# Kernel tuning notes

Measured on AMD Instinct MI355X. Metric: run time of the kernel, lower is better.

Reference implementation:

```python
import jax, jax.numpy as jnp
import numpy as np

VOCAB, D = 32000, 1024
EPS = 1e-5

def setup_inputs() -> dict:
    key = jax.random.key(0)
    k1, k2, k3, k4 = jax.random.split(key, 4)
    patch_embeddings = jax.random.normal(k1, (16, 256, D), dtype=jnp.float32)
    text_prototypes = jax.random.normal(k2, (VOCAB, D), dtype=jnp.float32) * 0.02
    # nn.Linear(d, d): weight [d, d], bias [d]
    lim = 1.0 / np.sqrt(D)
    W = jax.random.uniform(k3, (D, D), minval=-lim, maxval=lim, dtype=jnp.float32)
    b = jax.random.uniform(k4, (D,), minval=-lim, maxval=lim, dtype=jnp.float32)
    gamma = jnp.ones((D,), dtype=jnp.float32)
    beta = jnp.zeros((D,), dtype=jnp.float32)
    return {"patch_embeddings": patch_embeddings, "text_prototypes": text_prototypes,
            "W": W, "b": b, "gamma": gamma, "beta": beta}

def _layer_norm(x, gamma, beta):
    mu = jnp.mean(x, axis=-1, keepdims=True)
    var = jnp.mean(jnp.square(x - mu), axis=-1, keepdims=True)
    return (x - mu) * jax.lax.rsqrt(var + EPS) * gamma + beta

def reference(patch_embeddings, text_prototypes, W, b, gamma, beta):
    # similarities: [B, P, V]
    sims = jnp.einsum('bpd,vd->bpv', patch_embeddings, text_prototypes)
    attn = jax.nn.softmax(sims, axis=-1)
    reprogrammed = jnp.einsum('bpv,vd->bpd', attn, text_prototypes)
    transformed = jnp.einsum('bpd,ed->bpe', reprogrammed, W) + b
    return _layer_norm(patch_embeddings + transformed, gamma, beta)
```

## Files before the change

### kernel.cpp

```cpp
#include <hip/hip_runtime.h>
#include <hip/hip_bf16.h>
#include <cstdint>
#include <cstddef>

#define D_DIM 1024
#define VOCAB 32000
#define ROWS  4096

typedef __attribute__((ext_vector_type(8))) short bf16x8;
typedef __attribute__((ext_vector_type(4))) float f32x4;
typedef __attribute__((ext_vector_type(4))) int   i32x4;
typedef __attribute__((ext_vector_type(8))) int   i32x8;

static __device__ __forceinline__ i32x8 cat8(i32x4 lo, i32x4 hi) {
  return __builtin_shufflevector(lo, hi, 0, 1, 2, 3, 4, 5, 6, 7);
}

static __device__ __forceinline__ unsigned short f2bf(float f) {
  union { float f; unsigned int u; } c; c.f = f;
  unsigned int u = c.u;
  u += 0x7fffu + ((u >> 16) & 1u);
  return (unsigned short)(u >> 16);
}

static __device__ __forceinline__ int pk8(float a, float b) {
  return __builtin_amdgcn_cvt_pk_fp8_f32(a, b, 0, false);
}

static __device__ __forceinline__ void gload_lds16(const void* g, void* s) {
  __builtin_amdgcn_global_load_lds(
      (const __attribute__((address_space(1))) uint32_t*)(g),
      (__attribute__((address_space(3))) uint32_t*)(s), 16, 0, 0);
}

__global__ void k_cvt(const float* __restrict__ src, short* __restrict__ dst, int n4) {
  int i = blockIdx.x * 256 + threadIdx.x;
  if (i < n4) {
    float4 v = *(const float4*)(src + (size_t)i * 4);
    ushort4 u;
    u.x = f2bf(v.x); u.y = f2bf(v.y); u.z = f2bf(v.z); u.w = f2bf(v.w);
    *(ushort4*)(dst + (size_t)i * 4) = u;
  }
}

__global__ void k_cvt_q8(const float* __restrict__ src, uint8_t* __restrict__ dst) {
  int i = blockIdx.x * 256 + threadIdx.x;
  float4 a = *(const float4*)(src + (size_t)i * 8);
  float4 b = *(const float4*)(src + (size_t)i * 8 + 4);
  uint2 o;
  o.x = (pk8(a.x, a.y) & 0xffff) | (pk8(a.z, a.w) << 16);
  o.y = (pk8(b.x, b.y) & 0xffff) | (pk8(b.z, b.w) << 16);
  *(uint2*)(dst + (size_t)i * 8) = o;
}

__global__ void k_prep_K8(const float* __restrict__ src, uint8_t* __restrict__ kb,
                          uint8_t* __restrict__ kt, int R, int C) {
  __shared__ uint8_t tile[64][68];
  int t  = threadIdx.x;
  int r0 = blockIdx.x * 64;
  int c0 = blockIdx.y * 64;
  int lr = t >> 4;
  int lc = (t & 15) * 4;
#pragma unroll
  for (int i = 0; i < 4; ++i) {
    int r = lr + 16 * i;
    float4 v = *(const float4*)(src + (size_t)(r0 + r) * C + c0 + lc);
    unsigned p = (pk8(v.x * 64.f, v.y * 64.f) & 0xffff) | (pk8(v.z * 64.f, v.w * 64.f) << 16);
    *(unsigned*)&tile[r][lc] = p;
    *(unsigned*)(kb + (size_t)(r0 + r) * C + c0 + lc) = p;
  }
  __syncthreads();
#pragma unroll
  for (int i = 0; i < 4; ++i) {
    int c = lr + 16 * i;
    unsigned p = tile[lc + 0][c] | (tile[lc + 1][c] << 8) |
                 (tile[lc + 2][c] << 16) | ((unsigned)tile[lc + 3][c] << 24);
    *(unsigned*)(kt + (size_t)(c0 + c) * R + r0 + lc) = p;
  }
}

#define PS8 144
#define G1NT 8
__global__ __launch_bounds__(256, 2) void k_g1(
    const uint8_t* __restrict__ A,
    const uint8_t* __restrict__ B,
    uint8_t* __restrict__ Pout, float* __restrict__ den)
{
  __shared__ uint8_t smem[65536];

  int tid  = threadIdx.x;
  int wave = tid >> 6;
  int lane = tid & 63;
  int quad = lane >> 4;
  int t16  = lane & 15;
  int wy = wave >> 1, wx = wave & 1;

  int swz = (blockIdx.x & 7) * 1000 + (blockIdx.x >> 3);
  int nt  = swz >> 5;
  int mt  = swz & 31;
  long mBase = (long)mt * 128;
  long nBase = (long)nt * 128;

  const uint8_t* Ab = A + (size_t)mBase * D_DIM;
  const uint8_t* Bb = B + (size_t)nBase * D_DIM;
  int lrow = lane >> 3;
  int lcol = ((lane & 7) ^ lrow) * 16;

  f32x4 acc[4][4];
#pragma unroll
  for (int i = 0; i < 4; ++i)
#pragma unroll
    for (int j = 0; j < 4; ++j) acc[i][j] = (f32x4){0.f, 0.f, 0.f, 0.f};

  int sw  = t16 & 7;
  int co0 = (((quad << 1) ^ sw) << 4);
  const int SC1 = 0x7F7F7F7F;

  auto STAGE = [&](int slot, int t) {
    uint8_t* As = &smem[slot * 32768];
    uint8_t* Bs = As + 16384;
    int kk = t * 128;
#pragma unroll
    for (int i = 0; i < 4; ++i) {
      int row = wave * 32 + i * 8;
      gload_lds16(Ab + (size_t)(row + lrow) * D_DIM + kk + lcol, As + row * 128);
      gload_lds16(Bb + (size_t)(row + lrow) * D_DIM + kk + lcol, Bs + row * 128);
    }
  };

  STAGE(0, 0);
  STAGE(1, 1);

  for (int t = 0; t < G1NT; ++t) {
    const uint8_t* As = &smem[(t & 1) * 32768];
    const uint8_t* Bs = As + 16384;

    if (t + 1 < G1NT)
      asm volatile("s_waitcnt vmcnt(8)\n\ts_barrier" ::: "memory");
    else
      asm volatile("s_waitcnt vmcnt(0)\n\ts_barrier" ::: "memory");

    i32x8 af[4], bfr[4];
#pragma unroll
    for (int mi = 0; mi < 4; ++mi) {
      const uint8_t* rp = &As[(wy * 64 + mi * 16 + t16) * 128];
      af[mi] = cat8(*(const i32x4*)(rp + co0), *(const i32x4*)(rp + (co0 ^ 16)));
    }
#pragma unroll
    for (int ni = 0; ni < 4; ++ni) {
      const uint8_t* rp = &Bs[(wx * 64 + ni * 16 + t16) * 128];
      bfr[ni] = cat8(*(const i32x4*)(rp + co0), *(const i32x4*)(rp + (co0 ^ 16)));
    }
    __builtin_amdgcn_s_setprio(1);
#pragma unroll
    for (int mi = 0; mi < 4; ++mi)
#pragma unroll
      for (int ni = 0; ni < 4; ++ni)
        acc[mi][ni] = __builtin_amdgcn_mfma_scale_f32_16x16x128_f8f6f4(
            af[mi], bfr[ni], acc[mi][ni], 0, 0, 0, SC1, 0, SC1);
    __builtin_amdgcn_s_setprio(0);
    asm volatile("s_barrier" ::: "memory");
    if (t + 2 < G1NT) STAGE(t & 1, t + 2);
  }

  float rsum[4][4];
#pragma unroll
  for (int mi = 0; mi < 4; ++mi)
#pragma unroll
    for (int r = 0; r < 4; ++r) rsum[mi][r] = 0.f;
#pragma unroll
  for (int mi = 0; mi < 4; ++mi) {
    int rloc = wy * 64 + mi * 16 + quad * 4;
#pragma unroll
    for (int ni = 0; ni < 4; ++ni) {
      int cloc = wx * 64 + ni * 16 + t16;
#pragma unroll
      for (int r = 0; r < 4; ++r) {
        float e = __expf(acc[mi][ni][r] * 0.015625f);
        smem[(rloc + r) * PS8 + cloc] = (uint8_t)pk8(e, e);
        rsum[mi][r] += e;
      }
    }
  }
#pragma unroll
  for (int mi = 0; mi < 4; ++mi)
#pragma unroll
    for (int r = 0; r < 4; ++r) {
      float s = rsum[mi][r];
      s += __shfl_xor(s, 1);
      s += __shfl_xor(s, 2);
      s += __shfl_xor(s, 4);
      s += __shfl_xor(s, 8);
      if (t16 == 0)
        atomicAdd(&den[mBase + wy * 64 + mi * 16 + quad * 4 + r], s);
    }
  __syncthreads();
  int rr  = tid >> 3;
  int c16 = (tid & 7) * 16;
#pragma unroll
  for (int i = 0; i < 4; ++i) {
    int row = i * 32 + rr;
    i32x4 v = *(const i32x4*)&smem[row * PS8 + c16];
    *(i32x4*)&Pout[(size_t)(mBase + row) * VOCAB + nBase + c16] = v;
  }
}

#define G2NT 125
__global__ __launch_bounds__(512, 2) void k_g2(
    const uint8_t* __restrict__ P, const uint8_t* __restrict__ KT,
    float* __restrict__ n0, float* __restrict__ n1)
{
  __shared__ uint8_t smem[98304];

  int tid  = threadIdx.x;
  int wave = tid >> 6;
  int lane = tid & 63;
  int quad = lane >> 4;
  int t16  = lane & 15;
  int wm = wave >> 2;
  int wn = wave & 3;

  int xn = blockIdx.x & 3;
  int zz = (blockIdx.x >> 2) & 1;
  int ym = blockIdx.x >> 3;
  long mBase = (long)ym * 128;
  long nBase = (long)xn * 256;
  int  k0    = zz * 16000;

  const uint8_t* Ab = P  + (size_t)mBase * VOCAB + k0;
  const uint8_t* Bb = KT + (size_t)nBase * VOCAB + k0;
  int lrow = lane >> 3;
  int lcol = ((lane & 7) ^ lrow) * 16;

  f32x4 acc[4][4];
#pragma unroll
  for (int i = 0; i < 4; ++i)
#pragma unroll
    for (int j = 0; j < 4; ++j) acc[i][j] = (f32x4){0.f, 0.f, 0.f, 0.f};

  int sw  = t16 & 7;
  int co0 = (((quad << 1) ^ sw) << 4);
  const int SC1 = 0x7F7F7F7F;

  auto STAGE = [&](int slot, int t) {
    uint8_t* As = &smem[slot * 49152];
    uint8_t* Bs = As + 16384;
    long kk = (long)t * 128;
#pragma unroll
    for (int g = 0; g < 2; ++g) {
      int r0 = wave * 16 + g * 8;
      gload_lds16(Ab + (size_t)(r0 + lrow) * VOCAB + kk + lcol, As + r0 * 128);
    }
#pragma unroll
    for (int g = 0; g < 4; ++g) {
      int r0 = wave * 32 + g * 8;
      gload_lds16(Bb + (size_t)(r0 + lrow) * VOCAB + kk + lcol, Bs + r0 * 128);
    }
  };

  STAGE(0, 0);
  STAGE(1, 1);

  for (int t = 0; t < G2NT; ++t) {
    const uint8_t* As = &smem[(t & 1) * 49152];
    const uint8_t* Bs = As + 16384;

    if (t + 1 < G2NT)
      asm volatile("s_waitcnt vmcnt(6)\n\ts_barrier" ::: "memory");
    else
      asm volatile("s_waitcnt vmcnt(0)\n\ts_barrier" ::: "memory");

    i32x8 af[4], bfr[4];
#pragma unroll
    for (int mi = 0; mi < 4; ++mi) {
      const uint8_t* rp = As + (wm * 64 + mi * 16 + t16) * 128;
      af[mi] = cat8(*(const i32x4*)(rp + co0), *(const i32x4*)(rp + (co0 ^ 16)));
    }
#pragma unroll
    for (int ni = 0; ni < 4; ++ni) {
      const uint8_t* rp = Bs + (wn * 64 + ni * 16 + t16) * 128;
      bfr[ni] = cat8(*(const i32x4*)(rp + co0), *(const i32x4*)(rp + (co0 ^ 16)));
    }
    __builtin_amdgcn_s_setprio(1);
#pragma unroll
    for (int mi = 0; mi < 4; ++mi)
#pragma unroll
      for (int ni = 0; ni < 4; ++ni)
        acc[mi][ni] = __builtin_amdgcn_mfma_scale_f32_16x16x128_f8f6f4(
            af[mi], bfr[ni], acc[mi][ni], 0, 0, 0, SC1, 0, SC1);
    __builtin_amdgcn_s_setprio(0);
    asm volatile("s_barrier" ::: "memory");
    if (t + 2 < G2NT) STAGE(t & 1, t + 2);
  }

  float* outp = zz ? n1 : n0;
#pragma unroll
  for (int mi = 0; mi < 4; ++mi) {
    long row = mBase + wm * 64 + mi * 16 + quad * 4;
#pragma unroll
    for (int ni = 0; ni < 4; ++ni) {
      long col = nBase + wn * 64 + ni * 16 + t16;
#pragma unroll
      for (int r = 0; r < 4; ++r)
        __builtin_nontemporal_store(acc[mi][ni][r],
                                    &outp[(size_t)(row + r) * D_DIM + col]);
    }
  }
}

__global__ __launch_bounds__(256) void k_gemm_bf(
    const short* __restrict__ A, int lda,
    const short* __restrict__ B, int ldb, int Kdim,
    const float* __restrict__ bias, const float* __restrict__ resid,
    float* __restrict__ Cout)
{
  __shared__ short smem[16384];
  short* As = smem;
  short* Bs = smem + 8192;

  int tid  = threadIdx.x;
  int wave = tid >> 6;
  int lane = tid & 63;
  int quad = lane >> 4;
  int t16  = lane & 15;
  int wy = wave >> 1, wx = wave & 1;

  long mBase = (long)blockIdx.y * 128;
  long nBase = (long)blockIdx.x * 128;

  const short* Ab = A + (size_t)mBase * lda;
  const short* Bb = B + (size_t)nBase * ldb;
  int lrow = lane >> 3;
  int lcol = ((lane & 7) ^ lrow) * 8;

  f32x4 acc[4][4];
#pragma unroll
  for (int i = 0; i < 4; ++i)
#pragma unroll
    for (int j = 0; j < 4; ++j) acc[i][j] = (f32x4){0.f, 0.f, 0.f, 0.f};

  int sw = t16 & 7;

  for (int kk = 0; kk < Kdim; kk += 64) {
#pragma unroll
    for (int i = 0; i < 4; ++i) {
      int row = wave * 32 + i * 8;
      gload_lds16(Ab + (size_t)(row + lrow) * lda + kk + lcol, &As[row * 64]);
      gload_lds16(Bb + (size_t)(row + lrow) * ldb + kk + lcol, &Bs[row * 64]);
    }
    __syncthreads();
#pragma unroll
    for (int kc = 0; kc < 8; kc += 4) {
      bf16x8 af[4], bfr[4];
#pragma unroll
      for (int mi = 0; mi < 4; ++mi)
        af[mi] = *(const bf16x8*)&As[(wy * 64 + mi * 16 + t16) * 64 +
                                     (((kc + quad) ^ sw) << 3)];
#pragma unroll
      for (int ni = 0; ni < 4; ++ni)
        bfr[ni] = *(const bf16x8*)&Bs[(wx * 64 + ni * 16 + t16) * 64 +
                                      (((kc + quad) ^ sw) << 3)];
#pragma unroll
      for (int mi = 0; mi < 4; ++mi)
#pragma unroll
        for (int ni = 0; ni < 4; ++ni)
          acc[mi][ni] = __builtin_amdgcn_mfma_f32_16x16x32_bf16(af[mi], bfr[ni],
                                                                acc[mi][ni], 0, 0, 0);
    }
    __syncthreads();
  }

#pragma unroll
  for (int mi = 0; mi < 4; ++mi) {
    long row = mBase + wy * 64 + mi * 16 + quad * 4;
#pragma unroll
    for (int ni = 0; ni < 4; ++ni) {
      long col = nBase + wx * 64 + ni * 16 + t16;
#pragma unroll
      for (int r = 0; r < 4; ++r) {
        size_t idx = (size_t)(row + r) * 1024 + col;
        Cout[idx] = acc[mi][ni][r] + bias[col] + resid[idx];
      }
    }
  }
}

__global__ void k_div(const float* __restrict__ n0, const float* __restrict__ n1,
                      const float* __restrict__ den, short* __restrict__ out) {
  int i = (blockIdx.x * 256 + threadIdx.x) * 4;
  float4 a = *(const float4*)(n0 + i);
  float4 b = *(const float4*)(n1 + i);
  float inv = 0.015625f / den[i >> 10];
  ushort4 u;
  u.x = f2bf((a.x + b.x) * inv); u.y = f2bf((a.y + b.y) * inv);
  u.z = f2bf((a.z + b.z) * inv); u.w = f2bf((a.w + b.w) * inv);
  *(ushort4*)(out + i) = u;
}

__global__ __launch_bounds__(256) void k_ln(const float* __restrict__ x,
                                            const float* __restrict__ gamma,
                                            const float* __restrict__ beta,
                                            float* __restrict__ out) {
  __shared__ float s_sum[4], s_sq[4];
  int row = blockIdx.x;
  int tid = threadIdx.x;
  const float* xr = x + (size_t)row * 1024;
  float4 v = *(const float4*)(xr + tid * 4);
  float s = v.x + v.y + v.z + v.w;
  float q = v.x * v.x + v.y * v.y + v.z * v.z + v.w * v.w;
#pragma unroll
  for (int off = 32; off >= 1; off >>= 1) {
    s += __shfl_down(s, off);
    q += __shfl_down(q, off);
  }
  int wv = tid >> 6;
  if ((tid & 63) == 0) { s_sum[wv] = s; s_sq[wv] = q; }
  __syncthreads();
  float tot  = s_sum[0] + s_sum[1] + s_sum[2] + s_sum[3];
  float totq = s_sq[0] + s_sq[1] + s_sq[2] + s_sq[3];
  float mu   = tot * (1.0f / 1024.0f);
  float var  = totq * (1.0f / 1024.0f) - mu * mu;
  float rstd = rsqrtf(var + 1e-5f);
  float4 g = *(const float4*)(gamma + tid * 4);
  float4 b = *(const float4*)(beta + tid * 4);
  float4 o;
  o.x = (v.x - mu) * rstd * g.x + b.x;
  o.y = (v.y - mu) * rstd * g.y + b.y;
  o.z = (v.z - mu) * rstd * g.z + b.z;
  o.w = (v.w - mu) * rstd * g.w + b.w;
  *(float4*)(out + (size_t)row * 1024 + tid * 4) = o;
}

extern "C" void kernel_launch(void* const* d_in, const int* in_sizes, int n_in,
                              void* d_out, int out_size, void* d_ws, size_t ws_size,
                              hipStream_t stream) {
  const float* patch = (const float*)d_in[0];
  const float* proto = (const float*)d_in[1];
  const float* W     = (const float*)d_in[2];
  const float* bvec  = (const float*)d_in[3];
  const float* gamma = (const float*)d_in[4];
  const float* beta  = (const float*)d_in[5];
  float* out = (float*)d_out;

  char* ws = (char*)d_ws;
  size_t off = 0;
  uint8_t* Q8  = (uint8_t*)(ws + off); off += (size_t)ROWS * D_DIM;
  uint8_t* Kb8 = (uint8_t*)(ws + off); off += (size_t)VOCAB * D_DIM;
  uint8_t* KT8 = (uint8_t*)(ws + off); off += (size_t)VOCAB * D_DIM;
  short*   Wb  = (short*)(ws + off);   off += (size_t)D_DIM * D_DIM * 2;
  short*   Rb  = (short*)(ws + off);   off += (size_t)ROWS * D_DIM * 2;
  uint8_t* P8  = (uint8_t*)(ws + off); off += (size_t)ROWS * VOCAB;
  float*   num = (float*)(ws + off);   off += (size_t)ROWS * D_DIM * 4;
  float*   den = (float*)(ws + off);   off += (size_t)ROWS * 4;
  float*   pre = (float*)P8;
  float*   nz0 = (float*)Kb8;
  float*   nz1 = num;

  hipMemsetAsync(den, 0, ROWS * sizeof(float), stream);

  k_cvt_q8<<<ROWS * D_DIM / 8 / 256, 256, 0, stream>>>(patch, Q8);
  k_cvt<<<D_DIM * D_DIM / 4 / 256, 256, 0, stream>>>(W, Wb, D_DIM * D_DIM / 4);
  k_prep_K8<<<dim3(VOCAB / 64, D_DIM / 64), 256, 0, stream>>>(proto, Kb8, KT8, VOCAB, D_DIM);

  k_g1<<<8000, 256, 0, stream>>>(Q8, Kb8, P8, den);

  k_g2<<<256, 512, 0, stream>>>(P8, KT8, nz0, nz1);

  k_div<<<ROWS * D_DIM / 4 / 256, 256, 0, stream>>>(nz0, nz1, den, Rb);

  k_gemm_bf<<<dim3(D_DIM / 128, ROWS / 128), 256, 0, stream>>>(
      Rb, D_DIM, Wb, D_DIM, D_DIM, bvec, patch, pre);

  k_ln<<<ROWS, 256, 0, stream>>>(pre, gamma, beta, out);
}
```

Baseline: 647.6 us.

## Retile second GEMM to 128x128 blocks with 256 threads and 512 CTAs

The P·K^T GEMM moves from 128x256 tiles with 8 waves to 128x128 tiles with 4 waves, each wave still computing 64x64, and launches 512 blocks instead of 256. Block-index decomposition is reordered so split-K halves sit in the high bits and the D tiles are innermost. The aim is better occupancy and load balance across CUs with smaller LDS per block, at the cost of more global reloads of the A tile. Stores in k_g1's P output become nontemporal, and k_g2's output stores become regular.

Result: slower. 662.3 us (+2.3%).

```diff
diff --git a/kernel.cpp b/kernel.cpp
--- a/kernel.cpp
+++ b/kernel.cpp
@@ -201,34 +201,34 @@
   for (int i = 0; i < 4; ++i) {
     int row = i * 32 + rr;
     i32x4 v = *(const i32x4*)&smem[row * PS8 + c16];
-    *(i32x4*)&Pout[(size_t)(mBase + row) * VOCAB + nBase + c16] = v;
+    __builtin_nontemporal_store(v, (i32x4*)&Pout[(size_t)(mBase + row) * VOCAB + nBase + c16]);
   }
 }
 
 #define G2NT 125
-__global__ __launch_bounds__(512, 2) void k_g2(
+__global__ __launch_bounds__(256, 2) void k_g2(
     const uint8_t* __restrict__ P, const uint8_t* __restrict__ KT,
     float* __restrict__ n0, float* __restrict__ n1)
 {
-  __shared__ uint8_t smem[98304];
+  __shared__ uint8_t smem[65536];
 
   int tid  = threadIdx.x;
   int wave = tid >> 6;
   int lane = tid & 63;
   int quad = lane >> 4;
   int t16  = lane & 15;
-  int wm = wave >> 2;
-  int wn = wave & 3;
-
-  int xn = blockIdx.x & 3;
-  int zz = (blockIdx.x >> 2) & 1;
-  int ym = blockIdx.x >> 3;
-  long mBase = (long)ym * 128;
-  long nBase = (long)xn * 256;
+  int wy = wave >> 1, wx = wave & 1;
+
+  int bid = blockIdx.x;
+  int zz  = bid >> 8;
+  int dt  = bid & 7;
+  int mt  = (bid >> 3) & 31;
+  long mBase = (long)mt * 128;
+  long dBase = (long)dt * 128;
   int  k0    = zz * 16000;
 
   const uint8_t* Ab = P  + (size_t)mBase * VOCAB + k0;
-  const uint8_t* Bb = KT + (size_t)nBase * VOCAB + k0;
+  const uint8_t* Bb = KT + (size_t)dBase * VOCAB + k0;
   int lrow = lane >> 3;
   int lcol = ((lane & 7) ^ lrow) * 16;
 
@@ -243,18 +243,14 @@
   const int SC1 = 0x7F7F7F7F;
 
   auto STAGE = [&](int slot, int t) {
-    uint8_t* As = &smem[slot * 49152];
+    uint8_t* As = &smem[slot * 32768];
     uint8_t* Bs = As + 16384;
     long kk = (long)t * 128;
 #pragma unroll
-    for (int g = 0; g < 2; ++g) {
-      int r0 = wave * 16 + g * 8;
-      gload_lds16(Ab + (size_t)(r0 + lrow) * VOCAB + kk + lcol, As + r0 * 128);
-    }
-#pragma unroll
-    for (int g = 0; g < 4; ++g) {
-      int r0 = wave * 32 + g * 8;
-      gload_lds16(Bb + (size_t)(r0 + lrow) * VOCAB + kk + lcol, Bs + r0 * 128);
+    for (int i = 0; i < 4; ++i) {
+      int row = wave * 32 + i * 8;
+      gload_lds16(Ab + (size_t)(row + lrow) * VOCAB + kk + lcol, As + row * 128);
+      gload_lds16(Bb + (size_t)(row + lrow) * VOCAB + kk + lcol, Bs + row * 128);
     }
   };
 
@@ -262,23 +258,23 @@
   STAGE(1, 1);
 
   for (int t = 0; t < G2NT; ++t) {
-    const uint8_t* As = &smem[(t & 1) * 49152];
+    const uint8_t* As = &smem[(t & 1) * 32768];
     const uint8_t* Bs = As + 16384;
 
     if (t + 1 < G2NT)
-      asm volatile("s_waitcnt vmcnt(6)\n\ts_barrier" ::: "memory");
+      asm volatile("s_waitcnt vmcnt(8)\n\ts_barrier" ::: "memory");
     else
       asm volatile("s_waitcnt vmcnt(0)\n\ts_barrier" ::: "memory");
 
     i32x8 af[4], bfr[4];
 #pragma unroll
     for (int mi = 0; mi < 4; ++mi) {
-      const uint8_t* rp = As + (wm * 64 + mi * 16 + t16) * 128;
+      const uint8_t* rp = &As[(wy * 64 + mi * 16 + t16) * 128];
       af[mi] = cat8(*(const i32x4*)(rp + co0), *(const i32x4*)(rp + (co0 ^ 16)));
     }
 #pragma unroll
     for (int ni = 0; ni < 4; ++ni) {
-      const uint8_t* rp = Bs + (wn * 64 + ni * 16 + t16) * 128;
+      const uint8_t* rp = &Bs[(wx * 64 + ni * 16 + t16) * 128];
       bfr[ni] = cat8(*(const i32x4*)(rp + co0), *(const i32x4*)(rp + (co0 ^ 16)));
     }
     __builtin_amdgcn_s_setprio(1);
@@ -296,14 +292,13 @@
   float* outp = zz ? n1 : n0;
 #pragma unroll
   for (int mi = 0; mi < 4; ++mi) {
-    long row = mBase + wm * 64 + mi * 16 + quad * 4;
+    long row = mBase + wy * 64 + mi * 16 + quad * 4;
 #pragma unroll
     for (int ni = 0; ni < 4; ++ni) {
-      long col = nBase + wn * 64 + ni * 16 + t16;
+      long col = dBase + wx * 64 + ni * 16 + t16;
 #pragma unroll
       for (int r = 0; r < 4; ++r)
-        __builtin_nontemporal_store(acc[mi][ni][r],
-                                    &outp[(size_t)(row + r) * D_DIM + col]);
+        outp[(size_t)(row + r) * D_DIM + col] = acc[mi][ni][r];
     }
   }
 }
@@ -464,7 +459,7 @@
 
   k_g1<<<8000, 256, 0, stream>>>(Q8, Kb8, P8, den);
 
-  k_g2<<<256, 512, 0, stream>>>(P8, KT8, nz0, nz1);
+  k_g2<<<512, 256, 0, stream>>>(P8, KT8, nz0, nz1);
 
   k_div<<<ROWS * D_DIM / 4 / 256, 256, 0, stream>>>(nz0, nz1, den, Rb);
 
```

## Widen similarity GEMM tiles and switch both FP8 GEMMs to triple-buffered LDS

Applied to the files above, without the earlier changes.

The first FP8 GEMM now uses 512-thread blocks with 128x256 output tiles, halving the grid. Both FP8 GEMMs move from double to triple-buffered shared memory. The next stage is issued right after the wait barrier, which drops the trailing barrier each iteration. The probability tile is written with nontemporal stores, and the second GEMM's output stores become plain stores. This aims to overlap loads with MFMA work and cut barrier count, at the cost of 144KB LDS per block, limiting occupancy to one block per CU.

Measured after the change: 634.9 us. 1.02x faster.

```diff
diff --git a/kernel.cpp b/kernel.cpp
--- a/kernel.cpp
+++ b/kernel.cpp
@@ -79,27 +79,28 @@
   }
 }
 
-#define PS8 144
+#define PS1 272
 #define G1NT 8
-__global__ __launch_bounds__(256, 2) void k_g1(
+__global__ __launch_bounds__(512, 1) void k_g1(
     const uint8_t* __restrict__ A,
     const uint8_t* __restrict__ B,
     uint8_t* __restrict__ Pout, float* __restrict__ den)
 {
-  __shared__ uint8_t smem[65536];
+  __shared__ uint8_t smem[147456];
 
   int tid  = threadIdx.x;
   int wave = tid >> 6;
   int lane = tid & 63;
   int quad = lane >> 4;
   int t16  = lane & 15;
-  int wy = wave >> 1, wx = wave & 1;
-
-  int swz = (blockIdx.x & 7) * 1000 + (blockIdx.x >> 3);
+  int wm = wave >> 2;
+  int wn = wave & 3;
+
+  int swz = (blockIdx.x & 7) * 500 + (blockIdx.x >> 3);
   int nt  = swz >> 5;
   int mt  = swz & 31;
   long mBase = (long)mt * 128;
-  long nBase = (long)nt * 128;
+  long nBase = (long)nt * 256;
 
   const uint8_t* Ab = A + (size_t)mBase * D_DIM;
   const uint8_t* Bb = B + (size_t)nBase * D_DIM;
@@ -117,14 +118,18 @@
   const int SC1 = 0x7F7F7F7F;
 
   auto STAGE = [&](int slot, int t) {
-    uint8_t* As = &smem[slot * 32768];
+    uint8_t* As = &smem[slot * 49152];
     uint8_t* Bs = As + 16384;
     int kk = t * 128;
 #pragma unroll
-    for (int i = 0; i < 4; ++i) {
-      int row = wave * 32 + i * 8;
-      gload_lds16(Ab + (size_t)(row + lrow) * D_DIM + kk + lcol, As + row * 128);
-      gload_lds16(Bb + (size_t)(row + lrow) * D_DIM + kk + lcol, Bs + row * 128);
+    for (int g = 0; g < 2; ++g) {
+      int r0 = wave * 16 + g * 8;
+      gload_lds16(Ab + (size_t)(r0 + lrow) * D_DIM + kk + lcol, As + r0 * 128);
+    }
+#pragma unroll
+    for (int g = 0; g < 4; ++g) {
+      int r0 = wave * 32 + g * 8;
+      gload_lds16(Bb + (size_t)(r0 + lrow) * D_DIM + kk + lcol, Bs + r0 * 128);
     }
   };
 
@@ -132,23 +137,24 @@
   STAGE(1, 1);
 
   for (int t = 0; t < G1NT; ++t) {
-    const uint8_t* As = &smem[(t & 1) * 32768];
-    const uint8_t* Bs = As + 16384;
-
     if (t + 1 < G1NT)
-      asm volatile("s_waitcnt vmcnt(8)\n\ts_barrier" ::: "memory");
+      asm volatile("s_waitcnt vmcnt(6)\n\ts_barrier" ::: "memory");
     else
       asm volatile("s_waitcnt vmcnt(0)\n\ts_barrier" ::: "memory");
 
+    if (t + 2 < G1NT) STAGE((t + 2) % 3, t + 2);
+
+    const uint8_t* As = &smem[(t % 3) * 49152];
+    const uint8_t* Bs = As + 16384;
     i32x8 af[4], bfr[4];
 #pragma unroll
     for (int mi = 0; mi < 4; ++mi) {
-      const uint8_t* rp = &As[(wy * 64 + mi * 16 + t16) * 128];
+      const uint8_t* rp = &As[(wm * 64 + mi * 16 + t16) * 128];
       af[mi] = cat8(*(const i32x4*)(rp + co0), *(const i32x4*)(rp + (co0 ^ 16)));
     }
 #pragma unroll
     for (int ni = 0; ni < 4; ++ni) {
-      const uint8_t* rp = &Bs[(wx * 64 + ni * 16 + t16) * 128];
+      const uint8_t* rp = &Bs[(wn * 64 + ni * 16 + t16) * 128];
       bfr[ni] = cat8(*(const i32x4*)(rp + co0), *(const i32x4*)(rp + (co0 ^ 16)));
     }
     __builtin_amdgcn_s_setprio(1);
@@ -159,10 +165,9 @@
         acc[mi][ni] = __builtin_amdgcn_mfma_scale_f32_16x16x128_f8f6f4(
             af[mi], bfr[ni], acc[mi][ni], 0, 0, 0, SC1, 0, SC1);
     __builtin_amdgcn_s_setprio(0);
-    asm volatile("s_barrier" ::: "memory");
-    if (t + 2 < G1NT) STAGE(t & 1, t + 2);
-  }
-
+  }
+
+  __syncthreads();
   float rsum[4][4];
 #pragma unroll
   for (int mi = 0; mi < 4; ++mi)
@@ -170,14 +175,14 @@
     for (int r = 0; r < 4; ++r) rsum[mi][r] = 0.f;
 #pragma unroll
   for (int mi = 0; mi < 4; ++mi) {
-    int rloc = wy * 64 + mi * 16 + quad * 4;
+    int rloc = wm * 64 + mi * 16 + quad * 4;
 #pragma unroll
     for (int ni = 0; ni < 4; ++ni) {
-      int cloc = wx * 64 + ni * 16 + t16;
+      int cloc = wn * 64 + ni * 16 + t16;
 #pragma unroll
       for (int r = 0; r < 4; ++r) {
         float e = __expf(acc[mi][ni][r] * 0.015625f);
-        smem[(rloc + r) * PS8 + cloc] = (uint8_t)pk8(e, e);
+        smem[(rloc + r) * PS1 + cloc] = (uint8_t)pk8(e, e);
         rsum[mi][r] += e;
       }
     }
@@ -192,25 +197,25 @@
       s += __shfl_xor(s, 4);
       s += __shfl_xor(s, 8);
       if (t16 == 0)
-        atomicAdd(&den[mBase + wy * 64 + mi * 16 + quad * 4 + r], s);
+        atomicAdd(&den[mBase + wm * 64 + mi * 16 + quad * 4 + r], s);
     }
   __syncthreads();
-  int rr  = tid >> 3;
-  int c16 = (tid & 7) * 16;
+  int rr  = tid >> 4;
+  int c16 = (tid & 15) * 16;
 #pragma unroll
   for (int i = 0; i < 4; ++i) {
     int row = i * 32 + rr;
-    i32x4 v = *(const i32x4*)&smem[row * PS8 + c16];
-    *(i32x4*)&Pout[(size_t)(mBase + row) * VOCAB + nBase + c16] = v;
+    i32x4 v = *(const i32x4*)&smem[row * PS1 + c16];
+    __builtin_nontemporal_store(v, (i32x4*)&Pout[(size_t)(mBase + row) * VOCAB + nBase + c16]);
   }
 }
 
 #define G2NT 125
-__global__ __launch_bounds__(512, 2) void k_g2(
+__global__ __launch_bounds__(512, 1) void k_g2(
     const uint8_t* __restrict__ P, const uint8_t* __restrict__ KT,
     float* __restrict__ n0, float* __restrict__ n1)
 {
-  __shared__ uint8_t smem[98304];
+  __shared__ uint8_t smem[147456];
 
   int tid  = threadIdx.x;
   int wave = tid >> 6;
@@ -220,15 +225,16 @@
   int wm = wave >> 2;
   int wn = wave & 3;
 
-  int xn = blockIdx.x & 3;
-  int zz = (blockIdx.x >> 2) & 1;
-  int ym = blockIdx.x >> 3;
-  long mBase = (long)ym * 128;
-  long nBase = (long)xn * 256;
+  int bid = blockIdx.x;
+  int dt  = bid & 3;
+  int zz  = (bid >> 2) & 1;
+  int mt  = bid >> 3;
+  long mBase = (long)mt * 128;
+  long dBase = (long)dt * 256;
   int  k0    = zz * 16000;
 
   const uint8_t* Ab = P  + (size_t)mBase * VOCAB + k0;
-  const uint8_t* Bb = KT + (size_t)nBase * VOCAB + k0;
+  const uint8_t* Bb = KT + (size_t)dBase * VOCAB + k0;
   int lrow = lane >> 3;
   int lcol = ((lane & 7) ^ lrow) * 16;
 
@@ -262,23 +268,24 @@
   STAGE(1, 1);
 
   for (int t = 0; t < G2NT; ++t) {
-    const uint8_t* As = &smem[(t & 1) * 49152];
-    const uint8_t* Bs = As + 16384;
-
     if (t + 1 < G2NT)
       asm volatile("s_waitcnt vmcnt(6)\n\ts_barrier" ::: "memory");
     else
       asm volatile("s_waitcnt vmcnt(0)\n\ts_barrier" ::: "memory");
 
+    if (t + 2 < G2NT) STAGE((t + 2) % 3, t + 2);
+
+    const uint8_t* As = &smem[(t % 3) * 49152];
+    const uint8_t* Bs = As + 16384;
     i32x8 af[4], bfr[4];
 #pragma unroll
     for (int mi = 0; mi < 4; ++mi) {
-      const uint8_t* rp = As + (wm * 64 + mi * 16 + t16) * 128;
+      const uint8_t* rp = &As[(wm * 64 + mi * 16 + t16) * 128];
       af[mi] = cat8(*(const i32x4*)(rp + co0), *(const i32x4*)(rp + (co0 ^ 16)));
     }
 #pragma unroll
     for (int ni = 0; ni < 4; ++ni) {
-      const uint8_t* rp = Bs + (wn * 64 + ni * 16 + t16) * 128;
+      const uint8_t* rp = &Bs[(wn * 64 + ni * 16 + t16) * 128];
       bfr[ni] = cat8(*(const i32x4*)(rp + co0), *(const i32x4*)(rp + (co0 ^ 16)));
     }
     __builtin_amdgcn_s_setprio(1);
@@ -289,8 +296,6 @@
         acc[mi][ni] = __builtin_amdgcn_mfma_scale_f32_16x16x128_f8f6f4(
             af[mi], bfr[ni], acc[mi][ni], 0, 0, 0, SC1, 0, SC1);
     __builtin_amdgcn_s_setprio(0);
-    asm volatile("s_barrier" ::: "memory");
-    if (t + 2 < G2NT) STAGE(t & 1, t + 2);
   }
 
   float* outp = zz ? n1 : n0;
@@ -299,11 +304,10 @@
     long row = mBase + wm * 64 + mi * 16 + quad * 4;
 #pragma unroll
     for (int ni = 0; ni < 4; ++ni) {
-      long col = nBase + wn * 64 + ni * 16 + t16;
+      long col = dBase + wn * 64 + ni * 16 + t16;
 #pragma unroll
       for (int r = 0; r < 4; ++r)
-        __builtin_nontemporal_store(acc[mi][ni][r],
-                                    &outp[(size_t)(row + r) * D_DIM + col]);
+        outp[(size_t)(row + r) * D_DIM + col] = acc[mi][ni][r];
     }
   }
 }
@@ -462,7 +466,7 @@
   k_cvt<<<D_DIM * D_DIM / 4 / 256, 256, 0, stream>>>(W, Wb, D_DIM * D_DIM / 4);
   k_prep_K8<<<dim3(VOCAB / 64, D_DIM / 64), 256, 0, stream>>>(proto, Kb8, KT8, VOCAB, D_DIM);
 
-  k_g1<<<8000, 256, 0, stream>>>(Q8, Kb8, P8, den);
+  k_g1<<<4000, 512, 0, stream>>>(Q8, Kb8, P8, den);
 
   k_g2<<<256, 512, 0, stream>>>(P8, KT8, nz0, nz1);
 
```
